# Kernel tuning notes

Hardware: AMD Instinct MI355X
Metric: run time of the kernel (lower is better)

The kernel has to match this reference:

```python
import jax, jax.numpy as jnp
import numpy as np
import math
from itertools import combinations

SEQ_LEN = 8
D_MODEL = 2048
OUT_DIM = 1152
WAY = 5
SHOT = 5
N_SUPPORT = WAY * SHOT
N_QUERIES = 200
TUPLES = np.array(list(combinations(range(SEQ_LEN), 2)), dtype=np.int32)  # [28, 2]
L = TUPLES.shape[0]  # 28 temporal tuples
PE_SCALE = 0.1
LN_EPS = 1e-5
COS_EPS = 1e-8


def _pos_encoding(seq, d):
    pos = jnp.arange(seq, dtype=jnp.float32)[:, None]
    div = jnp.exp(jnp.arange(0, d, 2, dtype=jnp.float32) * (-math.log(10000.0) / d))
    pe = jnp.zeros((seq, d), dtype=jnp.float32)
    pe = pe.at[:, 0::2].set(jnp.sin(pos * div) * PE_SCALE)
    pe = pe.at[:, 1::2].set(jnp.cos(pos * div) * PE_SCALE)
    return pe  # [seq, d]


def _layernorm(x, g, b):
    mu = x.mean(-1, keepdims=True)
    var = ((x - mu) ** 2).mean(-1, keepdims=True)
    return (x - mu) * jax.lax.rsqrt(var + LN_EPS) * g + b


def setup_inputs() -> dict:
    key = jax.random.key(0)
    ks = jax.random.split(key, 6)
    support_set = jax.random.normal(ks[0], (N_SUPPORT, SEQ_LEN, D_MODEL), jnp.float32)
    queries = jax.random.normal(ks[1], (N_QUERIES, SEQ_LEN, D_MODEL), jnp.float32)
    # sorted equal-shot episode: labels = [0]*5 + [1]*5 + ... + [4]*5
    support_labels = jnp.repeat(jnp.arange(WAY, dtype=jnp.int32), SHOT)
    k_w = jax.random.normal(ks[2], (OUT_DIM, 2 * D_MODEL), jnp.float32) * 0.02
    v_w = jax.random.normal(ks[3], (OUT_DIM, 2 * D_MODEL), jnp.float32) * 0.02
    k_b = jnp.zeros((OUT_DIM,), jnp.float32)
    v_b = jnp.zeros((OUT_DIM,), jnp.float32)
    ln_k_g = jnp.ones((OUT_DIM,), jnp.float32)
    ln_k_b = jnp.zeros((OUT_DIM,), jnp.float32)
    return {"support_set": support_set, "support_labels": support_labels,
            "queries": queries, "k_w": k_w, "k_b": k_b, "v_w": v_w, "v_b": v_b,
            "ln_k_g": ln_k_g, "ln_k_b": ln_k_b}


def reference(support_set, support_labels, queries, k_w, k_b, v_w, v_b, ln_k_g, ln_k_b):
    # dropout is inference-mode (identity)
    pe = _pos_encoding(SEQ_LEN, D_MODEL)
    sp = support_set + pe  # [Ns, S, D_MODEL]
    qp = queries + pe      # [Nq, S, D_MODEL]

    tup = jnp.asarray(TUPLES)
    # gather temporal tuples: [N, L, 2, D_MODEL] -> [N, L, 2*D_MODEL]
    s_t = sp[:, tup].reshape(N_SUPPORT, L, 2 * D_MODEL)
    q_t = qp[:, tup].reshape(N_QUERIES, L, 2 * D_MODEL)

    ks_s = _layernorm(s_t @ k_w.T + k_b, ln_k_g, ln_k_b)  # [Ns, L, OUT]
    ks_q = _layernorm(q_t @ k_w.T + k_b, ln_k_g, ln_k_b)  # [Nq, L, OUT]
    vs_s = s_t @ v_w.T + v_b                               # [Ns, L, OUT] (no norm, per original)
    vs_q = q_t @ v_w.T + v_b                               # [Nq, L, OUT]

    # labels are sorted equal-shot -> group by class via reshape
    ks_c = ks_s.reshape(WAY, SHOT, L, OUT_DIM)
    vs_c = vs_s.reshape(WAY, SHOT, L, OUT_DIM)

    # attention scores: [WAY, Nq, L(query tuple), SHOT, L(support tuple)]
    scores = jnp.einsum('qld,wsed->wqlse', ks_q, ks_c) / math.sqrt(OUT_DIM)
    attn = jax.nn.softmax(scores.reshape(WAY, N_QUERIES, L, SHOT * L), axis=-1)
    attn = attn.reshape(WAY, N_QUERIES, L, SHOT, L)
    # prototype: sum over shot of attn @ class_v -> [WAY, Nq, L, OUT]
    proto = jnp.einsum('wqlse,wsed->wqld', attn, vs_c)

    # query logits: -||q_v - proto||_F^2 / L per class
    diff = vs_q[None] - proto  # [WAY, Nq, L, OUT]
    ori = (-(diff ** 2).sum(axis=(-2, -1)) / L).T  # [Nq, WAY]

    # all_distances_tensor [Nq, L*OUT, WAY]
    A = jnp.transpose(proto, (1, 2, 3, 0)).reshape(N_QUERIES, L * OUT_DIM, WAY)
    num = jnp.einsum('qda,qdb->qab', A, A)            # [Nq, WAY, WAY]
    nrm = jnp.sqrt((A * A).sum(axis=1))               # [Nq, WAY]
    den = jnp.maximum(nrm[:, :, None] * nrm[:, None, :], COS_EPS)
    sim = num / den                                    # [Nq, WAY, WAY]
    return sim, ori
```

## Files before the change

kernel.cpp:

```cpp
#include <hip/hip_runtime.h>
#include <hip/hip_bf16.h>
#include <math.h>

typedef __hip_bfloat16 bf16;
typedef short s16x8 __attribute__((ext_vector_type(8)));
typedef float f32x4 __attribute__((ext_vector_type(4)));

#define NQ 200
#define SEQ 8
#define DM 2048
#define OUTD 1152
#define LT 28
#define M_ALL 6300
#define SM 5600
#define SN_PAD 768
#define ATT_STRIDE 720
#define N2 2304
#define KP 160
#define ABLK 144

__device__ __forceinline__ float bf2f(bf16 v) { return __bfloat162float(v); }
__device__ __forceinline__ bf16 f2bf(float v) { return __float2bfloat16(v); }
__device__ __forceinline__ float ubits2f(unsigned int u16) {
    unsigned int i = u16 << 16;
    float f; __builtin_memcpy(&f, &i, 4); return f;
}
__device__ __forceinline__ unsigned short f2bits(float f) {
    bf16 b = __float2bfloat16(f);
    unsigned short u; __builtin_memcpy(&u, &b, 2); return u;
}

__device__ const int TUP_A[LT] = {0,0,0,0,0,0,0,1,1,1,1,1,1,2,2,2,2,2,3,3,3,3,4,4,4,5,5,6};
__device__ const int TUP_B[LT] = {1,2,3,4,5,6,7,2,3,4,5,6,7,3,4,5,6,7,4,5,6,7,5,6,7,6,7,7};

__global__ __launch_bounds__(256) void wconv2_k(const float4* __restrict__ kw,
                                                const float4* __restrict__ vw,
                                                ushort4* __restrict__ o,
                                                float* __restrict__ pe,
                                                bf16* __restrict__ attn_tail) {
    int i = blockIdx.x * 256 + threadIdx.x;
    float4 v = (i < 1179648) ? kw[i] : vw[i - 1179648];
    ushort4 r;
    r.x = f2bits(v.x); r.y = f2bits(v.y); r.z = f2bits(v.z); r.w = f2bits(v.w);
    o[i] = r;
    if (blockIdx.x < 64) {
        int p = blockIdx.x * 256 + threadIdx.x;
        int s = p >> 11, d = p & 2047;
        float dv = expf((float)(d & ~1) * (-9.210340371976184f / 2048.0f));
        float ang = (float)s * dv;
        pe[p] = (d & 1) ? cosf(ang) * 0.1f : sinf(ang) * 0.1f;
        for (int j = p; j < 32 * ATT_STRIDE; j += 64 * 256) attn_tail[j] = f2bf(0.f);
    }
}

__global__ __launch_bounds__(256) void pex_k(const float* __restrict__ sup,
                                             const float* __restrict__ qry,
                                             const float* __restrict__ pe,
                                             bf16* __restrict__ pexb) {
    int r = blockIdx.x, t = threadIdx.x;
    int n, s;
    const float* src;
    if (r < 200) { n = r >> 3; s = r & 7; src = sup; }
    else { int rr = r - 200; n = rr >> 3; s = rr & 7; src = qry; }
    const float4* row = (const float4*)(src + ((size_t)n * SEQ + s) * DM);
    const float4* per = (const float4*)(pe + (size_t)s * DM);
    ushort4* orow = (ushort4*)(pexb + (size_t)r * DM);
    for (int d = t; d < DM / 4; d += 256) {
        float4 a = row[d], p = per[d];
        ushort4 o;
        o.x = f2bits(a.x + p.x); o.y = f2bits(a.y + p.y);
        o.z = f2bits(a.z + p.z); o.w = f2bits(a.w + p.w);
        orow[d] = o;
    }
}

template <int TN>
__global__ __launch_bounds__(256) void gemm_bt(
    const bf16* __restrict__ A, int lda, size_t aZ,
    const bf16* __restrict__ B, int ldb, size_t bZ,
    float scale, bf16* __restrict__ C, int ldc, size_t cZ, int K, int mlim) {
    constexpr int JN = TN / 32;
    const int gx = gridDim.x, gy = gridDim.y;
    const int nwg = gx * gy * (int)gridDim.z;
    const int orig = ((int)blockIdx.z * gy + blockIdx.y) * gx + blockIdx.x;
    const int qc = nwg >> 3, rc = nwg & 7;
    const int xcd = orig & 7, sub = orig >> 3;
    const int lg = (xcd < rc ? xcd * (qc + 1) : rc * (qc + 1) + (xcd - rc) * qc) + sub;
    const int bx = lg % gx;
    const int rest = lg / gx;
    const int by = rest % gy, bz = rest / gy;

    const unsigned short* Ag0 = (const unsigned short*)A + aZ * bz;
    const unsigned short* Bg0 = (const unsigned short*)B + bZ * bz;
    const size_t cbase = cZ * bz;
    const int tile_m = bx * 128, tile_n = by * TN;
    __shared__ unsigned short As[4 * 128 * 8];
    __shared__ unsigned short Bs[4 * TN * 8];
    const int t = threadIdx.x, lane = t & 63, wave = t >> 6;
    const int wm = (wave & 1) * 64, wn = (wave >> 1) * (TN / 2);
    const int srow = t >> 1, sq0 = (t & 1) * 2;
    const unsigned short* Ag = Ag0 + (size_t)(tile_m + srow) * lda + (t & 1) * 16;
    unsigned short* AsW0 = &As[((sq0 + 0) * 128 + srow) * 8];
    unsigned short* AsW1 = &As[((sq0 + 1) * 128 + srow) * 8];
    const unsigned short* Bg;
    unsigned short* BsW0;
    unsigned short* BsW1 = nullptr;
    if constexpr (TN == 128) {
        Bg = Bg0 + (size_t)(tile_n + srow) * ldb + (t & 1) * 16;
        BsW0 = &Bs[((sq0 + 0) * 128 + srow) * 8];
        BsW1 = &Bs[((sq0 + 1) * 128 + srow) * 8];
    } else {
        Bg = Bg0 + (size_t)(tile_n + (t >> 2)) * ldb + (t & 3) * 8;
        BsW0 = &Bs[((t & 3) * 64 + (t >> 2)) * 8];
    }
    const int fr = lane & 15, quad = lane >> 4;

    f32x4 acc[4][JN];
#pragma unroll
    for (int i = 0; i < 4; i++)
#pragma unroll
        for (int j = 0; j < JN; j++) acc[i][j] = {0.f, 0.f, 0.f, 0.f};

    for (int k0 = 0; k0 < K; k0 += 32) {
        uint4 a0 = *(const uint4*)(Ag + k0);
        uint4 a1 = *(const uint4*)(Ag + k0 + 8);
        uint4 b0 = *(const uint4*)(Bg + k0);
        uint4 b1;
        if constexpr (TN == 128) b1 = *(const uint4*)(Bg + k0 + 8);
        __syncthreads();
        *(uint4*)AsW0 = a0; *(uint4*)AsW1 = a1;
        *(uint4*)BsW0 = b0;
        if constexpr (TN == 128) *(uint4*)BsW1 = b1;
        __syncthreads();
        s16x8 af[4], bfv[JN];
#pragma unroll
        for (int i = 0; i < 4; i++)
            af[i] = *(const s16x8*)&As[(quad * 128 + wm + i * 16 + fr) * 8];
#pragma unroll
        for (int j = 0; j < JN; j++)
            bfv[j] = *(const s16x8*)&Bs[(quad * TN + wn + j * 16 + fr) * 8];
#pragma unroll
        for (int i = 0; i < 4; i++)
#pragma unroll
            for (int j = 0; j < JN; j++)
                acc[i][j] = __builtin_amdgcn_mfma_f32_16x16x32_bf16(af[i], bfv[j], acc[i][j], 0, 0, 0);
    }

    const int rb = quad * 4;
#pragma unroll
    for (int i = 0; i < 4; i++)
#pragma unroll
        for (int j = 0; j < JN; j++) {
            const int col = tile_n + wn + j * 16 + fr;
#pragma unroll
            for (int r = 0; r < 4; r++) {
                const int row = tile_m + wm + i * 16 + rb + r;
                if (row < mlim)
                    C[cbase + (size_t)row * ldc + col] = f2bf(acc[i][j][r] * scale);
            }
        }
}

__global__ __launch_bounds__(256) void combine_kv(
    const unsigned int* __restrict__ Yk, const unsigned int* __restrict__ Yv,
    const float* __restrict__ kb, const float* __restrict__ vb,
    const float* __restrict__ lng, const float* __restrict__ lnb,
    bf16* __restrict__ ks, bf16* __restrict__ vs) {
    const int t = threadIdx.x, lane = t & 63, wave = t >> 6;
    int orig = blockIdx.x;
    const bool vpath = orig >= M_ALL;
    if (vpath) orig -= M_ALL;
    {
        const int qc = M_ALL >> 3, rc = M_ALL & 7;
        const int xcd = orig & 7, sub = orig >> 3;
        orig = (xcd < rc ? xcd * (qc + 1) : rc * (qc + 1) + (xcd - rc) * qc) + sub;
    }
    const int m = orig;
    int mm = m < 700 ? m : m - 700;
    int base = m < 700 ? 0 : 200;
    int nsamp = mm / LT, l = mm - nsamp * LT;
    const unsigned int* Y = vpath ? Yv : Yk;
    const uint4* ya4 = (const uint4*)(Y + (size_t)(base + nsamp * 8 + TUP_A[l]) * (N2 / 2));
    const uint4* yb4 = (const uint4*)(Y + (size_t)(base + nsamp * 8 + TUP_B[l]) * (N2 / 2));
    if (vpath) {
        const float4* vb4 = (const float4*)vb;
        for (int u = t; u < OUTD / 4; u += 256) {
            uint4 a4 = ya4[u], b4 = yb4[u];
            float4 c4 = vb4[u];
            ushort4 o;
            o.x = f2bits(ubits2f(a4.x & 0xFFFFu) + ubits2f(b4.x >> 16) + c4.x);
            o.y = f2bits(ubits2f(a4.y & 0xFFFFu) + ubits2f(b4.y >> 16) + c4.y);
            o.z = f2bits(ubits2f(a4.z & 0xFFFFu) + ubits2f(b4.z >> 16) + c4.z);
            o.w = f2bits(ubits2f(a4.w & 0xFFFFu) + ubits2f(b4.w >> 16) + c4.w);
            *(ushort4*)&vs[(size_t)m * OUTD + u * 4] = o;
        }
        return;
    }
    const float4* kb4 = (const float4*)kb;
    float vals[8];
    int cnt = 0;
    float s = 0.f, s2 = 0.f;
    for (int u = t; u < OUTD / 4; u += 256) {
        uint4 a4 = ya4[u], b4 = yb4[u];
        float4 c4 = kb4[u];
        float v0 = ubits2f(a4.x & 0xFFFFu) + ubits2f(b4.x >> 16) + c4.x;
        float v1 = ubits2f(a4.y & 0xFFFFu) + ubits2f(b4.y >> 16) + c4.y;
        float v2 = ubits2f(a4.z & 0xFFFFu) + ubits2f(b4.z >> 16) + c4.z;
        float v3 = ubits2f(a4.w & 0xFFFFu) + ubits2f(b4.w >> 16) + c4.w;
        vals[cnt] = v0; vals[cnt + 1] = v1; vals[cnt + 2] = v2; vals[cnt + 3] = v3;
        cnt += 4;
        s += (v0 + v1) + (v2 + v3);
        s2 += v0 * v0 + v1 * v1 + v2 * v2 + v3 * v3;
    }
    for (int o = 32; o > 0; o >>= 1) { s += __shfl_xor(s, o); s2 += __shfl_xor(s2, o); }
    __shared__ float r1[4], r2[4];
    if (lane == 0) { r1[wave] = s; r2[wave] = s2; }
    __syncthreads();
    s = r1[0] + r1[1] + r1[2] + r1[3];
    s2 = r2[0] + r2[1] + r2[2] + r2[3];
    float mu = s * (1.f / OUTD);
    float var = s2 * (1.f / OUTD) - mu * mu;
    float inv = rsqrtf(fmaxf(var, 0.f) + 1e-5f);
    const float4* lg4 = (const float4*)lng;
    const float4* lb4 = (const float4*)lnb;
    cnt = 0;
    for (int u = t; u < OUTD / 4; u += 256) {
        float4 g4 = lg4[u], b4v = lb4[u];
        ushort4 o;
        o.x = f2bits((vals[cnt]     - mu) * inv * g4.x + b4v.x);
        o.y = f2bits((vals[cnt + 1] - mu) * inv * g4.y + b4v.y);
        o.z = f2bits((vals[cnt + 2] - mu) * inv * g4.z + b4v.z);
        o.w = f2bits((vals[cnt + 3] - mu) * inv * g4.w + b4v.w);
        cnt += 4;
        *(ushort4*)&ks[(size_t)m * OUTD + u * 4] = o;
    }
}

__global__ __launch_bounds__(320) void sv_k(const bf16* __restrict__ sc,
                                            bf16* __restrict__ attn,
                                            const bf16* __restrict__ vs,
                                            bf16* __restrict__ vp,
                                            float* __restrict__ gbuf) {
    const int t = threadIdx.x;
    if (blockIdx.x < SM) {
        const int row = blockIdx.x, w = t >> 6, lane = t & 63;
        const bf16* src = sc + (size_t)row * SN_PAD + w * 140;
        bf16* dst = attn + (size_t)row * ATT_STRIDE + w * ABLK;
        float a = bf2f(src[lane]);
        float b = bf2f(src[lane + 64]);
        float c = (lane < 12) ? bf2f(src[lane + 128]) : -3.0e38f;
        float m = fmaxf(fmaxf(a, b), c);
        for (int o = 32; o > 0; o >>= 1) m = fmaxf(m, __shfl_xor(m, o));
        float ea = __expf(a - m), eb = __expf(b - m);
        float ec = (lane < 12) ? __expf(c - m) : 0.f;
        float s = ea + eb + ec;
        for (int o = 32; o > 0; o >>= 1) s += __shfl_xor(s, o);
        float inv = 1.f / s;
        dst[lane] = f2bf(ea * inv);
        dst[lane + 64] = f2bf(eb * inv);
        if (lane < 16) dst[lane + 128] = f2bf(lane < 12 ? ec * inv : 0.f);
        return;
    }
    const int vb = blockIdx.x - SM;
    if (vb == 0)
        for (int i = t; i < NQ * 21; i += 320) gbuf[i] = 0.f;
    int idx = vb * 320 + t;
    int j = idx % KP;
    int rest = idx / KP;
    int dcol = rest % OUTD;
    int w = rest / OUTD;
    vp[idx] = (j < 140) ? vs[(size_t)(w * 140 + j) * OUTD + dcol] : f2bf(0.f);
}

__global__ __launch_bounds__(256) void fproto_k(
    const bf16* __restrict__ attn,
    const bf16* __restrict__ vsp,
    const bf16* __restrict__ vs,
    float* __restrict__ gbuf) {
    const int nwg = gridDim.x;
    int orig = blockIdx.x;
    {
        const int qc = nwg >> 3, rc = nwg & 7;
        const int xcd = orig & 7, sub = orig >> 3;
        orig = (xcd < rc ? xcd * (qc + 1) : rc * (qc + 1) + (xcd - rc) * qc) + sub;
    }
    const int q = orig / 9, dt = orig - q * 9;
    const int t = threadIdx.x, lane = t & 63, wave = t >> 6;
    const int fr = lane & 15, quad = lane >> 4;

    __shared__ unsigned short As5[5 * 20 * 32 * 8];
    __shared__ float red[4][21];

    const unsigned short* attn_u = (const unsigned short*)attn;
    const unsigned short* vsp_u = (const unsigned short*)vsp;

    for (int slot = t; slot < 3200; slot += 256) {
        int w = slot / 640, rem = slot - w * 640;
        int kq = rem >> 5, row = rem & 31;
        *(uint4*)&As5[slot * 8] =
            *(const uint4*)&attn_u[(size_t)(q * 28 + row) * ATT_STRIDE + w * ABLK + kq * 8];
    }
    __syncthreads();

    f32x4 acc[5][2][2];
#pragma unroll
    for (int w = 0; w < 5; w++)
#pragma unroll
        for (int i = 0; i < 2; i++)
#pragma unroll
            for (int j = 0; j < 2; j++) acc[w][i][j] = {0.f, 0.f, 0.f, 0.f};

    const unsigned short* vbase =
        vsp_u + (size_t)(dt * 128 + wave * 32 + fr) * KP + quad * 8;

#pragma unroll
    for (int w = 0; w < 5; w++) {
        s16x8 bfv[5][2];
#pragma unroll
        for (int s = 0; s < 5; s++)
#pragma unroll
            for (int j = 0; j < 2; j++)
                bfv[s][j] = *(const s16x8*)(vbase
                    + (size_t)w * OUTD * KP + (size_t)j * 16 * KP + s * 32);
#pragma unroll
        for (int s = 0; s < 5; s++) {
            s16x8 af[2];
#pragma unroll
            for (int i = 0; i < 2; i++)
                af[i] = *(const s16x8*)&As5[(w * 640 + (s * 4 + quad) * 32 + i * 16 + fr) * 8];
#pragma unroll
            for (int i = 0; i < 2; i++)
#pragma unroll
                for (int j = 0; j < 2; j++)
                    acc[w][i][j] = __builtin_amdgcn_mfma_f32_16x16x32_bf16(af[i], bfv[s][j], acc[w][i][j], 0, 0, 0);
        }
    }

    float st[21];
#pragma unroll
    for (int k = 0; k < 21; k++) st[k] = 0.f;
#pragma unroll
    for (int i = 0; i < 2; i++)
#pragma unroll
        for (int r = 0; r < 4; r++) {
            const int l = i * 16 + quad * 4 + r;
            if (l < 28) {
                const size_t vrow = (size_t)(700 + q * 28 + l) * OUTD;
#pragma unroll
                for (int j = 0; j < 2; j++) {
                    const int col = dt * 128 + wave * 32 + j * 16 + fr;
                    float v = bf2f(vs[vrow + col]);
                    float pv[5];
#pragma unroll
                    for (int w = 0; w < 5; w++) pv[w] = acc[w][i][j][r];
                    st[20] += v * v;
                    int c = 0;
#pragma unroll
                    for (int a = 0; a < 5; a++) {
                        st[15 + a] += v * pv[a];
#pragma unroll
                        for (int b = a; b < 5; b++) st[c++] += pv[a] * pv[b];
                    }
                }
            }
        }
#pragma unroll
    for (int k = 0; k < 21; k++)
        for (int o = 32; o > 0; o >>= 1) st[k] += __shfl_xor(st[k], o);
    if (lane == 0)
#pragma unroll
        for (int k = 0; k < 21; k++) red[wave][k] = st[k];
    __syncthreads();
    if (t < 21)
        atomicAdd(&gbuf[q * 21 + t], red[0][t] + red[1][t] + red[2][t] + red[3][t]);
}

__global__ __launch_bounds__(64) void out_k(const float* __restrict__ gbuf,
                                            float* __restrict__ out) {
    int q = blockIdx.x;
    if (threadIdx.x != 0) return;
    const float* r = gbuf + q * 21;
    float G[5][5];
    int c = 0;
    for (int a = 0; a < 5; a++)
        for (int b = a; b < 5; b++) { G[a][b] = r[c]; G[b][a] = r[c]; c++; }
    float e = r[20];
    float nrm[5];
    for (int a = 0; a < 5; a++) nrm[a] = sqrtf(fmaxf(G[a][a], 0.f));
    for (int a = 0; a < 5; a++)
        for (int b = 0; b < 5; b++)
            out[(size_t)q * 25 + a * 5 + b] = G[a][b] / fmaxf(nrm[a] * nrm[b], 1e-8f);
    for (int w = 0; w < 5; w++)
        out[5000 + (size_t)q * 5 + w] = -(e - 2.f * r[15 + w] + G[w][w]) * (1.f / 28.f);
}

extern "C" void kernel_launch(void* const* d_in, const int* in_sizes, int n_in,
                              void* d_out, int out_size, void* d_ws, size_t ws_size,
                              hipStream_t stream) {
    const float* sup = (const float*)d_in[0];
    const float* qry = (const float*)d_in[2];
    const float* k_w = (const float*)d_in[3];
    const float* k_b = (const float*)d_in[4];
    const float* v_w = (const float*)d_in[5];
    const float* v_b = (const float*)d_in[6];
    const float* lng = (const float*)d_in[7];
    const float* lnb = (const float*)d_in[8];
    (void)in_sizes; (void)n_in; (void)out_size; (void)ws_size;

    char* ws = (char*)d_ws;
    bf16* pexb   = (bf16*)(ws + 0);
    bf16* wbf    = (bf16*)(ws + 7864320);
    bf16* Yk     = (bf16*)(ws + 26738688);
    bf16* Yv     = (bf16*)(ws + 35033088);
    bf16* ks     = (bf16*)(ws + 0);
    bf16* vs     = (bf16*)(ws + 16220160);
    bf16* sc     = (bf16*)(ws + 30735360);
    bf16* vsp    = (bf16*)(ws + 39386112);
    bf16* attn   = (bf16*)(ws + 41229312);
    float* gbuf  = (float*)(ws + 49339392);
    float* pe    = (float*)(ws + 49356192);

    wconv2_k<<<dim3(9216), dim3(256), 0, stream>>>(
        (const float4*)k_w, (const float4*)v_w, (ushort4*)wbf,
        pe, attn + (size_t)SM * ATT_STRIDE);
    pex_k<<<dim3(1800), dim3(256), 0, stream>>>(sup, qry, pe, pexb);

    gemm_bt<128><<<dim3(15, 18, 2), dim3(256), 0, stream>>>(
        pexb, DM, 0, wbf, DM, (size_t)4718592,
        1.0f, Yk, N2, (size_t)4147200, DM, 1800);

    combine_kv<<<dim3(2 * M_ALL), dim3(256), 0, stream>>>(
        (const unsigned int*)Yk, (const unsigned int*)Yv,
        k_b, v_b, lng, lnb, ks, vs);

    gemm_bt<64><<<dim3(44, 12, 1), dim3(256), 0, stream>>>(
        ks + (size_t)700 * OUTD, OUTD, 0, ks, OUTD, 0,
        0.029462782549439484f, sc, SN_PAD, 0, OUTD, 5632);

    sv_k<<<dim3(SM + 2880), dim3(320), 0, stream>>>(sc, attn, vs, vsp, gbuf);

    fproto_k<<<dim3(1800), dim3(256), 0, stream>>>(attn, vsp, vs, gbuf);

    out_k<<<dim3(NQ), dim3(64), 0, stream>>>(gbuf, (float*)d_out);
}
```

Before: 289.7 us.

## Fuse prep kernels with inline positional encoding and double GEMM K-step

Merges the weight-conversion and positional-encoding-add kernels into one launch and computes the sinusoidal encoding inline with fast intrinsics, so the pe buffer and its round trip through memory are gone. The bf16 GEMM now stages 64 K-elements per iteration instead of 32 and runs two MFMA sub-steps per pair of barriers, which halves the synchronisation count and doubles the LDS tile size. Fast __sinf/__cosf/__expf may differ slightly from the precise functions.

```diff
diff --git a/kernel.cpp b/kernel.cpp
--- a/kernel.cpp
+++ b/kernel.cpp
@@ -33,44 +33,46 @@
 __device__ const int TUP_A[LT] = {0,0,0,0,0,0,0,1,1,1,1,1,1,2,2,2,2,2,3,3,3,3,4,4,4,5,5,6};
 __device__ const int TUP_B[LT] = {1,2,3,4,5,6,7,2,3,4,5,6,7,3,4,5,6,7,4,5,6,7,5,6,7,6,7,7};
 
-__global__ __launch_bounds__(256) void wconv2_k(const float4* __restrict__ kw,
-                                                const float4* __restrict__ vw,
-                                                ushort4* __restrict__ o,
-                                                float* __restrict__ pe,
-                                                bf16* __restrict__ attn_tail) {
-    int i = blockIdx.x * 256 + threadIdx.x;
-    float4 v = (i < 1179648) ? kw[i] : vw[i - 1179648];
-    ushort4 r;
-    r.x = f2bits(v.x); r.y = f2bits(v.y); r.z = f2bits(v.z); r.w = f2bits(v.w);
-    o[i] = r;
-    if (blockIdx.x < 64) {
-        int p = blockIdx.x * 256 + threadIdx.x;
-        int s = p >> 11, d = p & 2047;
-        float dv = expf((float)(d & ~1) * (-9.210340371976184f / 2048.0f));
-        float ang = (float)s * dv;
-        pe[p] = (d & 1) ? cosf(ang) * 0.1f : sinf(ang) * 0.1f;
-        for (int j = p; j < 32 * ATT_STRIDE; j += 64 * 256) attn_tail[j] = f2bf(0.f);
-    }
-}
-
-__global__ __launch_bounds__(256) void pex_k(const float* __restrict__ sup,
-                                             const float* __restrict__ qry,
-                                             const float* __restrict__ pe,
-                                             bf16* __restrict__ pexb) {
-    int r = blockIdx.x, t = threadIdx.x;
+__global__ __launch_bounds__(256) void prep_k(const float4* __restrict__ kw,
+                                              const float4* __restrict__ vw,
+                                              ushort4* __restrict__ o,
+                                              const float* __restrict__ sup,
+                                              const float* __restrict__ qry,
+                                              bf16* __restrict__ pexb,
+                                              bf16* __restrict__ attn_tail) {
+    const int b = blockIdx.x, t = threadIdx.x;
+    if (b < 9216) {
+        int i = b * 256 + t;
+        float4 v = (i < 1179648) ? kw[i] : vw[i - 1179648];
+        ushort4 r;
+        r.x = f2bits(v.x); r.y = f2bits(v.y); r.z = f2bits(v.z); r.w = f2bits(v.w);
+        o[i] = r;
+        if (b < 64)
+            for (int j = b * 256 + t; j < 32 * ATT_STRIDE; j += 64 * 256)
+                attn_tail[j] = f2bf(0.f);
+        return;
+    }
+    const int r = b - 9216;
     int n, s;
     const float* src;
     if (r < 200) { n = r >> 3; s = r & 7; src = sup; }
     else { int rr = r - 200; n = rr >> 3; s = rr & 7; src = qry; }
     const float4* row = (const float4*)(src + ((size_t)n * SEQ + s) * DM);
-    const float4* per = (const float4*)(pe + (size_t)s * DM);
     ushort4* orow = (ushort4*)(pexb + (size_t)r * DM);
+    const float C = -9.210340371976184f / 2048.0f;
+    const float sf = (float)s;
     for (int d = t; d < DM / 4; d += 256) {
-        float4 a = row[d], p = per[d];
-        ushort4 o;
-        o.x = f2bits(a.x + p.x); o.y = f2bits(a.y + p.y);
-        o.z = f2bits(a.z + p.z); o.w = f2bits(a.w + p.w);
-        orow[d] = o;
+        float4 a = row[d];
+        float e0 = (float)(4 * d);
+        float dv0 = __expf(e0 * C);
+        float dv2 = __expf((e0 + 2.0f) * C);
+        float a0 = sf * dv0, a2 = sf * dv2;
+        ushort4 ov;
+        ov.x = f2bits(a.x + __sinf(a0) * 0.1f);
+        ov.y = f2bits(a.y + __cosf(a0) * 0.1f);
+        ov.z = f2bits(a.z + __sinf(a2) * 0.1f);
+        ov.w = f2bits(a.w + __cosf(a2) * 0.1f);
+        orow[d] = ov;
     }
 }
 
@@ -94,26 +96,25 @@
     const unsigned short* Bg0 = (const unsigned short*)B + bZ * bz;
     const size_t cbase = cZ * bz;
     const int tile_m = bx * 128, tile_n = by * TN;
-    __shared__ unsigned short As[4 * 128 * 8];
-    __shared__ unsigned short Bs[4 * TN * 8];
+    __shared__ unsigned short As[8 * 128 * 8];
+    __shared__ unsigned short Bs[8 * TN * 8];
     const int t = threadIdx.x, lane = t & 63, wave = t >> 6;
     const int wm = (wave & 1) * 64, wn = (wave >> 1) * (TN / 2);
-    const int srow = t >> 1, sq0 = (t & 1) * 2;
-    const unsigned short* Ag = Ag0 + (size_t)(tile_m + srow) * lda + (t & 1) * 16;
-    unsigned short* AsW0 = &As[((sq0 + 0) * 128 + srow) * 8];
-    unsigned short* AsW1 = &As[((sq0 + 1) * 128 + srow) * 8];
+    const int fr = lane & 15, quad = lane >> 4;
+
+    const int row0 = t & 127, kq0 = t >> 7;
+    const unsigned short* Ag = Ag0 + (size_t)(tile_m + row0) * lda + kq0 * 8;
+    unsigned short* AsW = &As[(kq0 * 128 + row0) * 8];
     const unsigned short* Bg;
-    unsigned short* BsW0;
-    unsigned short* BsW1 = nullptr;
+    unsigned short* BsW;
     if constexpr (TN == 128) {
-        Bg = Bg0 + (size_t)(tile_n + srow) * ldb + (t & 1) * 16;
-        BsW0 = &Bs[((sq0 + 0) * 128 + srow) * 8];
-        BsW1 = &Bs[((sq0 + 1) * 128 + srow) * 8];
+        Bg = Bg0 + (size_t)(tile_n + row0) * ldb + kq0 * 8;
+        BsW = &Bs[(kq0 * 128 + row0) * 8];
     } else {
-        Bg = Bg0 + (size_t)(tile_n + (t >> 2)) * ldb + (t & 3) * 8;
-        BsW0 = &Bs[((t & 3) * 64 + (t >> 2)) * 8];
-    }
-    const int fr = lane & 15, quad = lane >> 4;
+        const int brow = t & 63, bkq = t >> 6;
+        Bg = Bg0 + (size_t)(tile_n + brow) * ldb + bkq * 8;
+        BsW = &Bs[(bkq * 64 + brow) * 8];
+    }
 
     f32x4 acc[4][JN];
 #pragma unroll
@@ -121,29 +122,51 @@
 #pragma unroll
         for (int j = 0; j < JN; j++) acc[i][j] = {0.f, 0.f, 0.f, 0.f};
 
-    for (int k0 = 0; k0 < K; k0 += 32) {
+    for (int k0 = 0; k0 < K; k0 += 64) {
         uint4 a0 = *(const uint4*)(Ag + k0);
-        uint4 a1 = *(const uint4*)(Ag + k0 + 8);
-        uint4 b0 = *(const uint4*)(Bg + k0);
-        uint4 b1;
-        if constexpr (TN == 128) b1 = *(const uint4*)(Bg + k0 + 8);
+        uint4 a1 = *(const uint4*)(Ag + k0 + 16);
+        uint4 a2 = *(const uint4*)(Ag + k0 + 32);
+        uint4 a3 = *(const uint4*)(Ag + k0 + 48);
+        uint4 b0, b1, b2, b3;
+        if constexpr (TN == 128) {
+            b0 = *(const uint4*)(Bg + k0);
+            b1 = *(const uint4*)(Bg + k0 + 16);
+            b2 = *(const uint4*)(Bg + k0 + 32);
+            b3 = *(const uint4*)(Bg + k0 + 48);
+        } else {
+            b0 = *(const uint4*)(Bg + k0);
+            b1 = *(const uint4*)(Bg + k0 + 32);
+        }
         __syncthreads();
-        *(uint4*)AsW0 = a0; *(uint4*)AsW1 = a1;
-        *(uint4*)BsW0 = b0;
-        if constexpr (TN == 128) *(uint4*)BsW1 = b1;
+        *(uint4*)(AsW + 0)    = a0;
+        *(uint4*)(AsW + 2048) = a1;
+        *(uint4*)(AsW + 4096) = a2;
+        *(uint4*)(AsW + 6144) = a3;
+        if constexpr (TN == 128) {
+            *(uint4*)(BsW + 0)    = b0;
+            *(uint4*)(BsW + 2048) = b1;
+            *(uint4*)(BsW + 4096) = b2;
+            *(uint4*)(BsW + 6144) = b3;
+        } else {
+            *(uint4*)(BsW + 0)    = b0;
+            *(uint4*)(BsW + 2048) = b1;
+        }
         __syncthreads();
-        s16x8 af[4], bfv[JN];
-#pragma unroll
-        for (int i = 0; i < 4; i++)
-            af[i] = *(const s16x8*)&As[(quad * 128 + wm + i * 16 + fr) * 8];
-#pragma unroll
-        for (int j = 0; j < JN; j++)
-            bfv[j] = *(const s16x8*)&Bs[(quad * TN + wn + j * 16 + fr) * 8];
-#pragma unroll
-        for (int i = 0; i < 4; i++)
+#pragma unroll
+        for (int s = 0; s < 2; s++) {
+            s16x8 af[4], bfv[JN];
+#pragma unroll
+            for (int i = 0; i < 4; i++)
+                af[i] = *(const s16x8*)&As[((s * 4 + quad) * 128 + wm + i * 16 + fr) * 8];
 #pragma unroll
             for (int j = 0; j < JN; j++)
-                acc[i][j] = __builtin_amdgcn_mfma_f32_16x16x32_bf16(af[i], bfv[j], acc[i][j], 0, 0, 0);
+                bfv[j] = *(const s16x8*)&Bs[((s * 4 + quad) * TN + wn + j * 16 + fr) * 8];
+#pragma unroll
+            for (int i = 0; i < 4; i++)
+#pragma unroll
+                for (int j = 0; j < JN; j++)
+                    acc[i][j] = __builtin_amdgcn_mfma_f32_16x16x32_bf16(af[i], bfv[j], acc[i][j], 0, 0, 0);
+        }
     }
 
     const int rb = quad * 4;
@@ -418,12 +441,10 @@
     bf16* vsp    = (bf16*)(ws + 39386112);
     bf16* attn   = (bf16*)(ws + 41229312);
     float* gbuf  = (float*)(ws + 49339392);
-    float* pe    = (float*)(ws + 49356192);
-
-    wconv2_k<<<dim3(9216), dim3(256), 0, stream>>>(
+
+    prep_k<<<dim3(9216 + 1800), dim3(256), 0, stream>>>(
         (const float4*)k_w, (const float4*)v_w, (ushort4*)wbf,
-        pe, attn + (size_t)SM * ATT_STRIDE);
-    pex_k<<<dim3(1800), dim3(256), 0, stream>>>(sup, qry, pe, pexb);
+        sup, qry, pexb, attn + (size_t)SM * ATT_STRIDE);
 
     gemm_bt<128><<<dim3(15, 18, 2), dim3(256), 0, stream>>>(
         pexb, DM, 0, wbf, DM, (size_t)4718592,
```

Result: slower. 346.4 us (+19.6%).
